# Kernel tuning notes

Measured on AMD Instinct MI355X. Metric: run time of the kernel, lower is better.

Reference implementation:

```python
import jax, jax.numpy as jnp
import numpy as np

D = 768

def gru_cell(x, h, W_ih, W_hh, b_ih, b_hh):
    # torch.nn.GRUCell math
    gi = x @ W_ih.T + b_ih  # [*, 3D]
    gh = h @ W_hh.T + b_hh
    i_r, i_z, i_n = jnp.split(gi, 3, axis=-1)
    h_r, h_z, h_n = jnp.split(gh, 3, axis=-1)
    r = jax.nn.sigmoid(i_r + h_r)
    z = jax.nn.sigmoid(i_z + h_z)
    n = jnp.tanh(i_n + r * h_n)
    return (1.0 - z) * n + z * h


def setup_inputs() -> dict:
    key = jax.random.key(0)
    ks = jax.random.split(key, 16)
    S, E, N, R = 2048, 32768, 100000, 1000
    w = 0.05  # weight scale to avoid full gate saturation
    return {
        'encoder_output': jax.random.normal(ks[0], (1, D), jnp.float32),
        'sample_mask': jax.random.normal(ks[1], (S, D), jnp.float32),
        'seed_entities': jnp.arange(S, dtype=jnp.int64) if jax.config.jax_enable_x64 else jnp.arange(S, dtype=jnp.int32),
        'edge_heads': jax.random.randint(ks[2], (E,), 0, S),
        'edge_tails': jax.random.randint(ks[3], (E,), 0, N),
        'edge_type': jax.random.randint(ks[4], (E,), 0, R),
        'node2node': jnp.arange(N),
        'old_ndata': jnp.arange(N),
        'relation_embeddings': jax.random.normal(ks[5], (R, D), jnp.float32),
        'W_sub': jax.random.normal(ks[6], (D, D), jnp.float32) * w,
        'b_sub': jax.random.normal(ks[7], (D,), jnp.float32) * w,
        'W_obj': jax.random.normal(ks[8], (D, D), jnp.float32) * w,
        'b_obj': jax.random.normal(ks[9], (D,), jnp.float32) * w,
        'W_ih': jax.random.normal(ks[10], (3 * D, D), jnp.float32) * w,
        'W_hh': jax.random.normal(ks[11], (3 * D, D), jnp.float32) * w,
        'b_ih': jax.random.normal(ks[12], (3 * D,), jnp.float32) * w,
        'b_hh': jax.random.normal(ks[13], (3 * D,), jnp.float32) * w,
        'default_ndata': jax.random.normal(ks[14], (N, D), jnp.float32),  # stands in for torch.randn(768) fill
    }


def reference(encoder_output, sample_mask, seed_entities, edge_heads, edge_tails,
              edge_type, node2node, old_ndata, relation_embeddings,
              W_sub, b_sub, W_obj, b_obj, W_ih, W_hh, b_ih, b_hh, default_ndata):
    S = seed_entities.shape[0]
    E = edge_heads.shape[0]
    N = old_ndata.shape[0]

    # per-seed: sub_embedding = tanh(Linear(sample_mask[i])); r0 = GRUCell(encoder_output, sub)
    sub = jnp.tanh(sample_mask @ W_sub.T + b_sub)                    # [S, D]
    x0 = jnp.broadcast_to(encoder_output, sub.shape)                 # [S, D]
    r0 = gru_cell(x0, sub, W_ih, W_hh, b_ih, b_hh)                   # [S, D]

    # map node id -> seed position (for write-order timestamps)
    seed_pos_of_node = jnp.full((N,), -1, jnp.int32).at[seed_entities].set(
        jnp.arange(S, dtype=jnp.int32))
    edge_seed_pos = seed_pos_of_node[edge_heads]                     # [E]

    # per-edge: rj = GRUCell(r0[head], rel_emb); obj = tanh(Linear(rj))
    rel = relation_embeddings[edge_type]                             # [E, D]
    rj = gru_cell(r0[edge_heads], rel, W_ih, W_hh, b_ih, b_hh)       # [E, D]
    obj = jnp.tanh(rj @ W_obj.T + b_obj)                             # [E, D]

    # writes happen in order seed0, seed0-edges, seed1, seed1-edges, ...
    stride = jnp.int32(E + 1)
    seed_t = jnp.arange(S, dtype=jnp.int32) * stride                 # seed write times
    edge_t = edge_seed_pos * stride + 1 + jnp.arange(E, dtype=jnp.int32)

    best = jnp.full((N,), -1, jnp.int32)
    best = best.at[seed_entities].max(seed_t)
    best = best.at[edge_tails].max(edge_t)

    win_s = best[seed_entities] == seed_t
    win_e = best[edge_tails] == edge_t

    table = jnp.zeros((N, sub.shape[-1]), sub.dtype)
    table = table.at[jnp.where(win_s, seed_entities, N)].set(sub, mode='drop')
    table = table.at[jnp.where(win_e, edge_tails, N)].set(obj, mode='drop')

    ids = node2node[old_ndata]                                       # reindexed node ids
    written = best[ids] >= 0
    return jnp.where(written[:, None], table[ids], default_ndata)    # [N, D]
```

## Files before the change

kernel.cpp:

```cpp
#include <hip/hip_runtime.h>

#define D 768
#define D3 2304

typedef __bf16 bf16x8 __attribute__((ext_vector_type(8)));
typedef float f32x4 __attribute__((ext_vector_type(4)));

__device__ __forceinline__ float b2f(unsigned short u) {
    unsigned int i = ((unsigned int)u) << 16;
    return __builtin_bit_cast(float, i);
}
__device__ __forceinline__ unsigned short f2b(float f) {
    unsigned int i = __builtin_bit_cast(unsigned int, f);
    i += 0x7FFFu + ((i >> 16) & 1u);
    return (unsigned short)(i >> 16);
}
__device__ __forceinline__ float sigm(float x) { return 1.0f / (1.0f + __expf(-x)); }

__global__ void k_cast(const float* __restrict__ in, unsigned short* __restrict__ out, int n)
{
    int i4 = (blockIdx.x * blockDim.x + threadIdx.x) * 4;
    if (i4 >= n) return;
    float4 v = *(const float4*)(in + i4);
    ushort4 u;
    u.x = f2b(v.x); u.y = f2b(v.y); u.z = f2b(v.z); u.w = f2b(v.w);
    *(ushort4*)(out + i4) = u;
}

template<int ACT, bool OBF>
__global__ __launch_bounds__(256)
void gemm_nt(const unsigned short* __restrict__ A,
             const unsigned short* __restrict__ B,
             const float* __restrict__ bias,
             void* __restrict__ Cv,
             int M, int N, int K)
{
    constexpr int BM = 64, BN = 64, BK = 32;
    __shared__ __align__(16) unsigned short As[BM * BK];
    __shared__ __align__(16) unsigned short Bs[BN * BK];

    const int bm   = blockIdx.y * BM;
    const int bn   = blockIdx.x * BN;
    const int tid  = threadIdx.x;
    const int wave = tid >> 6;
    const int lane = tid & 63;

    const int srow = tid >> 2;
    const int scol = (tid & 3) << 3;

    int arow = bm + srow; if (arow >= M) arow = M - 1;
    int brow = bn + srow; if (brow >= N) brow = N - 1;
    const unsigned short* Ap = A + (size_t)arow * K + scol;
    const unsigned short* Bp = B + (size_t)brow * K + scol;
    unsigned short* AsP = &As[srow * BK + scol];
    unsigned short* BsP = &Bs[srow * BK + scol];

    const int fr = lane & 15;
    const int fk = (lane >> 4) << 3;

    f32x4 acc[4];
#pragma unroll
    for (int i = 0; i < 4; ++i) acc[i] = (f32x4)0.0f;

    for (int k0 = 0; k0 < K; k0 += BK) {
        *(uint4*)AsP = *(const uint4*)(Ap + k0);
        *(uint4*)BsP = *(const uint4*)(Bp + k0);
        __syncthreads();
        bf16x8 a = *(const bf16x8*)&As[(wave * 16 + fr) * BK + fk];
#pragma unroll
        for (int ct = 0; ct < 4; ++ct) {
            bf16x8 b = *(const bf16x8*)&Bs[(ct * 16 + fr) * BK + fk];
            acc[ct] = __builtin_amdgcn_mfma_f32_16x16x32_bf16(a, b, acc[ct], 0, 0, 0);
        }
        __syncthreads();
    }

    const int rbase = bm + wave * 16 + ((lane >> 4) << 2);
#pragma unroll
    for (int ct = 0; ct < 4; ++ct) {
        int col = bn + ct * 16 + (lane & 15);
        if (col >= N) continue;
        float bv = bias ? bias[col] : 0.0f;
#pragma unroll
        for (int r = 0; r < 4; ++r) {
            int row = rbase + r;
            if (row < M) {
                float v = acc[ct][r] + bv;
                if (ACT == 1) v = tanhf(v);
                if (OBF) ((unsigned short*)Cv)[(size_t)row * N + col] = f2b(v);
                else     ((float*)Cv)[(size_t)row * N + col] = v;
            }
        }
    }
}

__global__ void k_gi0(const float* __restrict__ enc,
                      const float* __restrict__ Wih,
                      const float* __restrict__ bih,
                      float* __restrict__ gi0)
{
    int j = blockIdx.x * 4 + (threadIdx.x >> 6);
    int lane = threadIdx.x & 63;
    if (j >= D3) return;
    const float* w = Wih + (size_t)j * D;
    float s = 0.0f;
    for (int k = lane; k < D; k += 64) s += enc[k] * w[k];
#pragma unroll
    for (int off = 32; off > 0; off >>= 1) s += __shfl_xor(s, off, 64);
    if (lane == 0) gi0[j] = s + bih[j];
}

__global__ void k_r0(const float* __restrict__ gi0, const float* __restrict__ gh,
                     const unsigned short* __restrict__ sub,
                     unsigned short* __restrict__ r0, int S)
{
    int idx = blockIdx.x * blockDim.x + threadIdx.x;
    if (idx >= S * D) return;
    int s = idx / D, d = idx - s * D;
    const float* g = gh + (size_t)s * D3;
    float r = sigm(gi0[d] + g[d]);
    float z = sigm(gi0[D + d] + g[D + d]);
    float n = tanhf(gi0[2 * D + d] + r * g[2 * D + d]);
    float h = b2f(sub[idx]);
    r0[idx] = f2b((1.0f - z) * n + z * h);
}

__global__ void k_edge(const int* __restrict__ heads, const int* __restrict__ types,
                       const float* __restrict__ Gi, const float* __restrict__ Ghr,
                       const float* __restrict__ rel,
                       unsigned short* __restrict__ rj, int E)
{
    int idx = blockIdx.x * blockDim.x + threadIdx.x;
    if (idx >= E * D) return;
    int e = idx / D, d = idx - e * D;
    int hd = heads[e], t = types[e];
    const float* gi = Gi + (size_t)hd * D3;
    const float* gh = Ghr + (size_t)t * D3;
    float r = sigm(gi[d] + gh[d]);
    float z = sigm(gi[D + d] + gh[D + d]);
    float n = tanhf(gi[2 * D + d] + r * gh[2 * D + d]);
    float h = rel[(size_t)t * D + d];
    rj[idx] = f2b((1.0f - z) * n + z * h);
}

__global__ void k_seed_st(const int* __restrict__ se, int* __restrict__ seed_pos,
                          int* __restrict__ best, int S, int stride)
{
    int s = blockIdx.x * blockDim.x + threadIdx.x;
    if (s >= S) return;
    int node = se[s];
    atomicMax(&seed_pos[node], s);
    atomicMax(&best[node], s * stride);
}

__global__ void k_edge_time(const int* __restrict__ heads, const int* __restrict__ tails,
                            const int* __restrict__ seed_pos, int* __restrict__ best,
                            int E, int stride)
{
    int e = blockIdx.x * blockDim.x + threadIdx.x;
    if (e >= E) return;
    int p = seed_pos[heads[e]];
    int t = p * stride + 1 + e;
    if (t < 0) return;
    atomicMax(&best[tails[e]], t);
}

__global__ void k_seed_win(const int* __restrict__ se, const int* __restrict__ best,
                           int* __restrict__ winner, int S, int stride)
{
    int s = blockIdx.x * blockDim.x + threadIdx.x;
    if (s >= S) return;
    int node = se[s];
    if (best[node] == s * stride) winner[node] = s;
}

__global__ void k_edge_win(const int* __restrict__ heads, const int* __restrict__ tails,
                           const int* __restrict__ seed_pos, const int* __restrict__ best,
                           int* __restrict__ winner, int E, int S, int stride)
{
    int e = blockIdx.x * blockDim.x + threadIdx.x;
    if (e >= E) return;
    int p = seed_pos[heads[e]];
    int t = p * stride + 1 + e;
    if (t < 0) return;
    int node = tails[e];
    if (best[node] == t) winner[node] = S + e;
}

__global__ void k_out(const int* __restrict__ n2n, const int* __restrict__ oldnd,
                      const int* __restrict__ best, const int* __restrict__ winner,
                      const unsigned short* __restrict__ sub,
                      const unsigned short* __restrict__ obj,
                      const float* __restrict__ defnd,
                      float* __restrict__ out, int N, int S)
{
    int idx = blockIdx.x * blockDim.x + threadIdx.x;
    const int JP = D / 4;
    if (idx >= N * JP) return;
    int i = idx / JP, j = idx - i * JP;
    int id = n2n[oldnd[i]];
    float4 v;
    if (best[id] >= 0) {
        int w = winner[id];
        const unsigned short* src = (w < S) ? sub + (size_t)w * D + j * 4
                                            : obj + (size_t)(w - S) * D + j * 4;
        ushort4 u = *(const ushort4*)src;
        v.x = b2f(u.x); v.y = b2f(u.y); v.z = b2f(u.z); v.w = b2f(u.w);
    } else {
        v = *(const float4*)(defnd + (size_t)i * D + j * 4);
    }
    *(float4*)(out + (size_t)i * D + j * 4) = v;
}

extern "C" void kernel_launch(void* const* d_in, const int* in_sizes, int n_in,
                              void* d_out, int out_size, void* d_ws, size_t ws_size,
                              hipStream_t stream)
{
    const float* enc    = (const float*)d_in[0];
    const float* smask  = (const float*)d_in[1];
    const int* seed_ent = (const int*)d_in[2];
    const int* eheads   = (const int*)d_in[3];
    const int* etails   = (const int*)d_in[4];
    const int* etype    = (const int*)d_in[5];
    const int* n2n      = (const int*)d_in[6];
    const int* oldnd    = (const int*)d_in[7];
    const float* rel    = (const float*)d_in[8];
    const float* Wsub   = (const float*)d_in[9];
    const float* bsub   = (const float*)d_in[10];
    const float* Wobj   = (const float*)d_in[11];
    const float* bobj   = (const float*)d_in[12];
    const float* Wih    = (const float*)d_in[13];
    const float* Whh    = (const float*)d_in[14];
    const float* bih    = (const float*)d_in[15];
    const float* bhh    = (const float*)d_in[16];
    const float* defnd  = (const float*)d_in[17];

    const int S = in_sizes[2];
    const int E = in_sizes[3];
    const int N = in_sizes[6];
    const int R = in_sizes[8] / D;
    const int stride = E + 1;

    char* p = (char*)d_ws;
    auto carve = [&](size_t bytes) -> char* {
        char* r = p; p += (bytes + 255) & ~(size_t)255; return r;
    };
    unsigned short* smask_b = (unsigned short*)carve((size_t)S * D * 2);
    unsigned short* Wsub_b  = (unsigned short*)carve((size_t)D * D * 2);
    unsigned short* Wobj_b  = (unsigned short*)carve((size_t)D * D * 2);
    unsigned short* Wih_b   = (unsigned short*)carve((size_t)D3 * D * 2);
    unsigned short* Whh_b   = (unsigned short*)carve((size_t)D3 * D * 2);
    unsigned short* rel_b   = (unsigned short*)carve((size_t)R * D * 2);
    unsigned short* sub     = (unsigned short*)carve((size_t)S * D * 2);
    unsigned short* r0      = (unsigned short*)carve((size_t)S * D * 2);
    unsigned short* rj      = (unsigned short*)carve((size_t)E * D * 2);
    unsigned short* obj     = (unsigned short*)carve((size_t)E * D * 2);
    float* gi0 = (float*)carve((size_t)D3 * 4);
    float* gh  = (float*)carve((size_t)S * D3 * 4);
    float* ghr = (float*)carve((size_t)R * D3 * 4);
    int* seed_pos = (int*)carve((size_t)N * 4);
    int* best     = (int*)carve((size_t)N * 4);
    int* winner   = (int*)carve((size_t)N * 4);

    dim3 blk(256);
    auto g1 = [](int n) { return dim3((n + 255) / 256); };

    hipMemsetAsync(seed_pos, 0xFF, (size_t)N * 4, stream);
    hipMemsetAsync(best,     0xFF, (size_t)N * 4, stream);
    hipMemsetAsync(winner,   0xFF, (size_t)N * 4, stream);

    k_cast<<<g1(S * D / 4),  blk, 0, stream>>>(smask, smask_b, S * D);
    k_cast<<<g1(D * D / 4),  blk, 0, stream>>>(Wsub,  Wsub_b,  D * D);
    k_cast<<<g1(D * D / 4),  blk, 0, stream>>>(Wobj,  Wobj_b,  D * D);
    k_cast<<<g1(D3 * D / 4), blk, 0, stream>>>(Wih,   Wih_b,   D3 * D);
    k_cast<<<g1(D3 * D / 4), blk, 0, stream>>>(Whh,   Whh_b,   D3 * D);
    k_cast<<<g1(R * D / 4),  blk, 0, stream>>>(rel,   rel_b,   R * D);

    gemm_nt<1, true><<<dim3(D / 64, (S + 63) / 64), blk, 0, stream>>>(
        smask_b, Wsub_b, bsub, sub, S, D, D);
    k_gi0<<<dim3((D3 + 3) / 4), blk, 0, stream>>>(enc, Wih, bih, gi0);
    gemm_nt<0, false><<<dim3(D3 / 64, (S + 63) / 64), blk, 0, stream>>>(
        sub, Whh_b, bhh, gh, S, D3, D);
    k_r0<<<g1(S * D), blk, 0, stream>>>(gi0, gh, sub, r0, S);
    gemm_nt<0, false><<<dim3(D3 / 64, (S + 63) / 64), blk, 0, stream>>>(
        r0, Wih_b, bih, gh, S, D3, D);
    gemm_nt<0, false><<<dim3(D3 / 64, (R + 63) / 64), blk, 0, stream>>>(
        rel_b, Whh_b, bhh, ghr, R, D3, D);
    k_edge<<<g1(E * D), blk, 0, stream>>>(eheads, etype, gh, ghr, rel, rj, E);
    gemm_nt<1, true><<<dim3(D / 64, (E + 63) / 64), blk, 0, stream>>>(
        rj, Wobj_b, bobj, obj, E, D, D);

    k_seed_st<<<g1(S), blk, 0, stream>>>(seed_ent, seed_pos, best, S, stride);
    k_edge_time<<<g1(E), blk, 0, stream>>>(eheads, etails, seed_pos, best, E, stride);
    k_seed_win<<<g1(S), blk, 0, stream>>>(seed_ent, best, winner, S, stride);
    k_edge_win<<<g1(E), blk, 0, stream>>>(eheads, etails, seed_pos, best, winner, E, S, stride);

    k_out<<<g1(N * (D / 4)), blk, 0, stream>>>(
        n2n, oldnd, best, winner, sub, obj, defnd, (float*)d_out, N, S);
}
```

Before: 886.0 us.

## Compute edge GRU and obj GEMM only for winning edges; use 128x128 GEMM tiles

Moves the last-write-wins winner computation ahead of the edge work and compacts the winning edges into a dense list with an atomic counter. Only those edges then go through the GRU elementwise step and the W_obj GEMM, whose row count is read from device memory. The GEMM is also retiled to 128x128 blocks with a 4x4 MFMA register tile per wave and direct global-to-LDS loads. This adds a compaction kernel, a row indirection in the output kernel, and grids sized for the worst case that exit early when a block has no rows.

```diff
diff --git a/kernel.cpp b/kernel.cpp
--- a/kernel.cpp
+++ b/kernel.cpp
@@ -16,6 +16,13 @@
     return (unsigned short)(i >> 16);
 }
 __device__ __forceinline__ float sigm(float x) { return 1.0f / (1.0f + __expf(-x)); }
+
+typedef __attribute__((address_space(1))) const unsigned int* as1p;
+typedef __attribute__((address_space(3))) unsigned int* as3p;
+__device__ __forceinline__ void glds16(const unsigned short* g, unsigned short* l)
+{
+    __builtin_amdgcn_global_load_lds((as1p)g, (as3p)l, 16, 0, 0);
+}
 
 __global__ void k_cast(const float* __restrict__ in, unsigned short* __restrict__ out, int n)
 {
@@ -29,66 +36,93 @@
 
 template<int ACT, bool OBF>
 __global__ __launch_bounds__(256)
-void gemm_nt(const unsigned short* __restrict__ A,
-             const unsigned short* __restrict__ B,
-             const float* __restrict__ bias,
-             void* __restrict__ Cv,
-             int M, int N, int K)
-{
-    constexpr int BM = 64, BN = 64, BK = 32;
-    __shared__ __align__(16) unsigned short As[BM * BK];
-    __shared__ __align__(16) unsigned short Bs[BN * BK];
-
-    const int bm   = blockIdx.y * BM;
-    const int bn   = blockIdx.x * BN;
+void gemm_nt128(const unsigned short* __restrict__ A,
+                const unsigned short* __restrict__ B,
+                const float* __restrict__ bias,
+                void* __restrict__ Cv,
+                int M, const int* __restrict__ Mptr,
+                int N, int K)
+{
+    if (Mptr) M = *Mptr;
+    const int bm = blockIdx.y * 128;
+    if (bm >= M) return;
+    const int bn = blockIdx.x * 128;
+    constexpr int BK = 32;
+
+    __shared__ __align__(16) unsigned short As[128 * BK];
+    __shared__ __align__(16) unsigned short Bs[128 * BK];
+
     const int tid  = threadIdx.x;
     const int wave = tid >> 6;
     const int lane = tid & 63;
-
-    const int srow = tid >> 2;
-    const int scol = (tid & 3) << 3;
-
-    int arow = bm + srow; if (arow >= M) arow = M - 1;
-    int brow = bn + srow; if (brow >= N) brow = N - 1;
-    const unsigned short* Ap = A + (size_t)arow * K + scol;
-    const unsigned short* Bp = B + (size_t)brow * K + scol;
-    unsigned short* AsP = &As[srow * BK + scol];
-    unsigned short* BsP = &Bs[srow * BK + scol];
+    const int wr = wave >> 1, wc = wave & 1;
+
+    const int c0 = wave * 2;
+    const int sr = lane >> 2;
+    const int sc = (lane & 3) << 3;
+
+    int ra0 = bm + c0 * 16 + sr;         if (ra0 >= M) ra0 = M - 1;
+    int ra1 = bm + (c0 + 1) * 16 + sr;   if (ra1 >= M) ra1 = M - 1;
+    int rb0 = bn + c0 * 16 + sr;         if (rb0 >= N) rb0 = N - 1;
+    int rb1 = bn + (c0 + 1) * 16 + sr;   if (rb1 >= N) rb1 = N - 1;
+
+    const unsigned short* Ag0 = A + (size_t)ra0 * K + sc;
+    const unsigned short* Ag1 = A + (size_t)ra1 * K + sc;
+    const unsigned short* Bg0 = B + (size_t)rb0 * K + sc;
+    const unsigned short* Bg1 = B + (size_t)rb1 * K + sc;
+    unsigned short* Al0 = &As[c0 * 512];
+    unsigned short* Al1 = &As[(c0 + 1) * 512];
+    unsigned short* Bl0 = &Bs[c0 * 512];
+    unsigned short* Bl1 = &Bs[(c0 + 1) * 512];
 
     const int fr = lane & 15;
     const int fk = (lane >> 4) << 3;
-
-    f32x4 acc[4];
-#pragma unroll
-    for (int i = 0; i < 4; ++i) acc[i] = (f32x4)0.0f;
+    const unsigned short* AsF = &As[(wr * 64 + fr) * BK + fk];
+    const unsigned short* BsF = &Bs[(wc * 64 + fr) * BK + fk];
+
+    f32x4 acc[4][4];
+#pragma unroll
+    for (int m = 0; m < 4; ++m)
+#pragma unroll
+        for (int n = 0; n < 4; ++n) acc[m][n] = (f32x4)0.0f;
 
     for (int k0 = 0; k0 < K; k0 += BK) {
-        *(uint4*)AsP = *(const uint4*)(Ap + k0);
-        *(uint4*)BsP = *(const uint4*)(Bp + k0);
+        glds16(Ag0 + k0, Al0);
+        glds16(Ag1 + k0, Al1);
+        glds16(Bg0 + k0, Bl0);
+        glds16(Bg1 + k0, Bl1);
         __syncthreads();
-        bf16x8 a = *(const bf16x8*)&As[(wave * 16 + fr) * BK + fk];
-#pragma unroll
-        for (int ct = 0; ct < 4; ++ct) {
-            bf16x8 b = *(const bf16x8*)&Bs[(ct * 16 + fr) * BK + fk];
-            acc[ct] = __builtin_amdgcn_mfma_f32_16x16x32_bf16(a, b, acc[ct], 0, 0, 0);
-        }
+        bf16x8 a[4], b[4];
+#pragma unroll
+        for (int m = 0; m < 4; ++m) a[m] = *(const bf16x8*)(AsF + m * 16 * BK);
+#pragma unroll
+        for (int n = 0; n < 4; ++n) b[n] = *(const bf16x8*)(BsF + n * 16 * BK);
+#pragma unroll
+        for (int m = 0; m < 4; ++m)
+#pragma unroll
+            for (int n = 0; n < 4; ++n)
+                acc[m][n] = __builtin_amdgcn_mfma_f32_16x16x32_bf16(a[m], b[n], acc[m][n], 0, 0, 0);
         __syncthreads();
     }
 
-    const int rbase = bm + wave * 16 + ((lane >> 4) << 2);
-#pragma unroll
-    for (int ct = 0; ct < 4; ++ct) {
-        int col = bn + ct * 16 + (lane & 15);
-        if (col >= N) continue;
-        float bv = bias ? bias[col] : 0.0f;
-#pragma unroll
-        for (int r = 0; r < 4; ++r) {
-            int row = rbase + r;
-            if (row < M) {
-                float v = acc[ct][r] + bv;
-                if (ACT == 1) v = tanhf(v);
-                if (OBF) ((unsigned short*)Cv)[(size_t)row * N + col] = f2b(v);
-                else     ((float*)Cv)[(size_t)row * N + col] = v;
+    const int rr = (lane >> 4) << 2;
+    const int cc = lane & 15;
+#pragma unroll
+    for (int m = 0; m < 4; ++m) {
+        const int row = bm + wr * 64 + m * 16 + rr;
+#pragma unroll
+        for (int n = 0; n < 4; ++n) {
+            const int col = bn + wc * 64 + n * 16 + cc;
+            if (col >= N) continue;
+            const float bv = bias ? bias[col] : 0.0f;
+#pragma unroll
+            for (int r = 0; r < 4; ++r) {
+                if (row + r < M) {
+                    float v = acc[m][n][r] + bv;
+                    if (ACT == 1) v = tanhf(v);
+                    if (OBF) ((unsigned short*)Cv)[(size_t)(row + r) * N + col] = f2b(v);
+                    else     ((float*)Cv)[(size_t)(row + r) * N + col] = v;
+                }
             }
         }
     }
@@ -125,24 +159,6 @@
     r0[idx] = f2b((1.0f - z) * n + z * h);
 }
 
-__global__ void k_edge(const int* __restrict__ heads, const int* __restrict__ types,
-                       const float* __restrict__ Gi, const float* __restrict__ Ghr,
-                       const float* __restrict__ rel,
-                       unsigned short* __restrict__ rj, int E)
-{
-    int idx = blockIdx.x * blockDim.x + threadIdx.x;
-    if (idx >= E * D) return;
-    int e = idx / D, d = idx - e * D;
-    int hd = heads[e], t = types[e];
-    const float* gi = Gi + (size_t)hd * D3;
-    const float* gh = Ghr + (size_t)t * D3;
-    float r = sigm(gi[d] + gh[d]);
-    float z = sigm(gi[D + d] + gh[D + d]);
-    float n = tanhf(gi[2 * D + d] + r * gh[2 * D + d]);
-    float h = rel[(size_t)t * D + d];
-    rj[idx] = f2b((1.0f - z) * n + z * h);
-}
-
 __global__ void k_seed_st(const int* __restrict__ se, int* __restrict__ seed_pos,
                           int* __restrict__ best, int S, int stride)
 {
@@ -187,8 +203,67 @@
     if (best[node] == t) winner[node] = S + e;
 }
 
+__global__ void k_compact(const int* __restrict__ best, const int* __restrict__ winner,
+                          int* __restrict__ cnt, int* __restrict__ wedge,
+                          int* __restrict__ objrow, int N, int S)
+{
+    int n = blockIdx.x * blockDim.x + threadIdx.x;
+    if (n >= N) return;
+    int w = winner[n];
+    if (best[n] >= 0 && w >= S) {
+        int r = atomicAdd(cnt, 1);
+        wedge[r] = w - S;
+        objrow[n] = r;
+    }
+}
+
+__global__ void k_edge2(const int* __restrict__ wedge, const int* __restrict__ cntp,
+                        const int* __restrict__ heads, const int* __restrict__ types,
+                        const float* __restrict__ Gi, const float* __restrict__ Ghr,
+                        const float* __restrict__ rel,
+                        unsigned short* __restrict__ rjw)
+{
+    const int W = *cntp;
+    const int wave = threadIdx.x >> 6;
+    const int lane = threadIdx.x & 63;
+    for (int row = blockIdx.x * 4 + wave; row < W; row += gridDim.x * 4) {
+        int e = wedge[row];
+        int hd = heads[e], t = types[e];
+        const float* gi = Gi + (size_t)hd * D3;
+        const float* gh = Ghr + (size_t)t * D3;
+        const float* rl = rel + (size_t)t * D;
+        unsigned short* out = rjw + (size_t)row * D;
+#pragma unroll
+        for (int i = 0; i < 3; ++i) {
+            int d = i * 256 + lane * 4;
+            float4 vr = *(const float4*)(gi + d);
+            float4 hr = *(const float4*)(gh + d);
+            float4 vz = *(const float4*)(gi + D + d);
+            float4 hz = *(const float4*)(gh + D + d);
+            float4 vn = *(const float4*)(gi + 2 * D + d);
+            float4 hn = *(const float4*)(gh + 2 * D + d);
+            float4 hh = *(const float4*)(rl + d);
+            ushort4 o;
+            { float r = sigm(vr.x + hr.x), z = sigm(vz.x + hz.x);
+              float n = tanhf(vn.x + r * hn.x);
+              o.x = f2b((1.0f - z) * n + z * hh.x); }
+            { float r = sigm(vr.y + hr.y), z = sigm(vz.y + hz.y);
+              float n = tanhf(vn.y + r * hn.y);
+              o.y = f2b((1.0f - z) * n + z * hh.y); }
+            { float r = sigm(vr.z + hr.z), z = sigm(vz.z + hz.z);
+              float n = tanhf(vn.z + r * hn.z);
+              o.z = f2b((1.0f - z) * n + z * hh.z); }
+            { float r = sigm(vr.w + hr.w), z = sigm(vz.w + hz.w);
+              float n = tanhf(vn.w + r * hn.w);
+              o.w = f2b((1.0f - z) * n + z * hh.w); }
+            *(ushort4*)(out + d) = o;
+        }
+    }
+}
+
 __global__ void k_out(const int* __restrict__ n2n, const int* __restrict__ oldnd,
                       const int* __restrict__ best, const int* __restrict__ winner,
+                      const int* __restrict__ objrow,
                       const unsigned short* __restrict__ sub,
                       const unsigned short* __restrict__ obj,
                       const float* __restrict__ defnd,
@@ -203,7 +278,7 @@
     if (best[id] >= 0) {
         int w = winner[id];
         const unsigned short* src = (w < S) ? sub + (size_t)w * D + j * 4
-                                            : obj + (size_t)(w - S) * D + j * 4;
+                                            : obj + (size_t)objrow[id] * D + j * 4;
         ushort4 u = *(const ushort4*)src;
         v.x = b2f(u.x); v.y = b2f(u.y); v.z = b2f(u.z); v.w = b2f(u.w);
     } else {
@@ -240,6 +315,7 @@
     const int N = in_sizes[6];
     const int R = in_sizes[8] / D;
     const int stride = E + 1;
+    const int maxW = (E < N) ? E : N;
 
     char* p = (char*)d_ws;
     auto carve = [&](size_t bytes) -> char* {
@@ -253,21 +329,32 @@
     unsigned short* rel_b   = (unsigned short*)carve((size_t)R * D * 2);
     unsigned short* sub     = (unsigned short*)carve((size_t)S * D * 2);
     unsigned short* r0      = (unsigned short*)carve((size_t)S * D * 2);
-    unsigned short* rj      = (unsigned short*)carve((size_t)E * D * 2);
-    unsigned short* obj     = (unsigned short*)carve((size_t)E * D * 2);
+    unsigned short* rj      = (unsigned short*)carve((size_t)maxW * D * 2);
+    unsigned short* obj     = (unsigned short*)carve((size_t)maxW * D * 2);
     float* gi0 = (float*)carve((size_t)D3 * 4);
     float* gh  = (float*)carve((size_t)S * D3 * 4);
     float* ghr = (float*)carve((size_t)R * D3 * 4);
     int* seed_pos = (int*)carve((size_t)N * 4);
     int* best     = (int*)carve((size_t)N * 4);
     int* winner   = (int*)carve((size_t)N * 4);
+    int* wedge    = (int*)carve((size_t)maxW * 4);
+    int* objrow   = (int*)carve((size_t)N * 4);
+    int* cnt      = (int*)carve(256);
 
     dim3 blk(256);
     auto g1 = [](int n) { return dim3((n + 255) / 256); };
+    auto gemmg = [](int M, int N_) { return dim3(N_ / 128, (M + 127) / 128); };
 
     hipMemsetAsync(seed_pos, 0xFF, (size_t)N * 4, stream);
     hipMemsetAsync(best,     0xFF, (size_t)N * 4, stream);
     hipMemsetAsync(winner,   0xFF, (size_t)N * 4, stream);
+    hipMemsetAsync(cnt,      0x00, 4, stream);
+
+    k_seed_st  <<<g1(S), blk, 0, stream>>>(seed_ent, seed_pos, best, S, stride);
+    k_edge_time<<<g1(E), blk, 0, stream>>>(eheads, etails, seed_pos, best, E, stride);
+    k_seed_win <<<g1(S), blk, 0, stream>>>(seed_ent, best, winner, S, stride);
+    k_edge_win <<<g1(E), blk, 0, stream>>>(eheads, etails, seed_pos, best, winner, E, S, stride);
+    k_compact  <<<g1(N), blk, 0, stream>>>(best, winner, cnt, wedge, objrow, N, S);
 
     k_cast<<<g1(S * D / 4),  blk, 0, stream>>>(smask, smask_b, S * D);
     k_cast<<<g1(D * D / 4),  blk, 0, stream>>>(Wsub,  Wsub_b,  D * D);
@@ -276,25 +363,21 @@
     k_cast<<<g1(D3 * D / 4), blk, 0, stream>>>(Whh,   Whh_b,   D3 * D);
     k_cast<<<g1(R * D / 4),  blk, 0, stream>>>(rel,   rel_b,   R * D);
 
-    gemm_nt<1, true><<<dim3(D / 64, (S + 63) / 64), blk, 0, stream>>>(
-        smask_b, Wsub_b, bsub, sub, S, D, D);
+    gemm_nt128<1, true><<<gemmg(S, D), blk, 0, stream>>>(
+        smask_b, Wsub_b, bsub, sub, S, nullptr, D, D);
     k_gi0<<<dim3((D3 + 3) / 4), blk, 0, stream>>>(enc, Wih, bih, gi0);
-    gemm_nt<0, false><<<dim3(D3 / 64, (S + 63) / 64), blk, 0, stream>>>(
-        sub, Whh_b, bhh, gh, S, D3, D);
+    gemm_nt128<0, false><<<gemmg(S, D3), blk, 0, stream>>>(
+        sub, Whh_b, bhh, gh, S, nullptr, D3, D);
     k_r0<<<g1(S * D), blk, 0, stream>>>(gi0, gh, sub, r0, S);
-    gemm_nt<0, false><<<dim3(D3 / 64, (S + 63) / 64), blk, 0, stream>>>(
-        r0, Wih_b, bih, gh, S, D3, D);
-    gemm_nt<0, false><<<dim3(D3 / 64, (R + 63) / 64), blk, 0, stream>>>(
-        rel_b, Whh_b, bhh, ghr, R, D3, D);
-    k_edge<<<g1(E * D), blk, 0, stream>>>(eheads, etype, gh, ghr, rel, rj, E);
-    gemm_nt<1, true><<<dim3(D / 64, (E + 63) / 64), blk, 0, stream>>>(
-        rj, Wobj_b, bobj, obj, E, D, D);
-
-    k_seed_st<<<g1(S), blk, 0, stream>>>(seed_ent, seed_pos, best, S, stride);
-    k_edge_time<<<g1(E), blk, 0, stream>>>(eheads, etails, seed_pos, best, E, stride);
-    k_seed_win<<<g1(S), blk, 0, stream>>>(seed_ent, best, winner, S, stride);
-    k_edge_win<<<g1(E), blk, 0, stream>>>(eheads, etails, seed_pos, best, winner, E, S, stride);
+    gemm_nt128<0, false><<<gemmg(S, D3), blk, 0, stream>>>(
+        r0, Wih_b, bih, gh, S, nullptr, D3, D);
+    gemm_nt128<0, false><<<gemmg(R, D3), blk, 0, stream>>>(
+        rel_b, Whh_b, bhh, ghr, R, nullptr, D3, D);
+
+    k_edge2<<<dim3(2048), blk, 0, stream>>>(wedge, cnt, eheads, etype, gh, ghr, rel, rj);
+    gemm_nt128<1, true><<<gemmg(maxW, D), blk, 0, stream>>>(
+        rj, Wobj_b, bobj, obj, maxW, cnt, D, D);
 
     k_out<<<g1(N * (D / 4)), blk, 0, stream>>>(
-        n2n, oldnd, best, winner, sub, obj, defnd, (float*)d_out, N, S);
-}
+        n2n, oldnd, best, winner, objrow, sub, obj, defnd, (float*)d_out, N, S);
+}
```

New measurement: 909.9 us. 1.03x slower.
